# Performance work log

Hardware: AMD Instinct MI355X
Metric: run time of the kernel (lower is better)

## Reference

```python
import jax, jax.numpy as jnp
import numpy as np

BETA = 0.95      # leak
THRESH = 1.0     # snntorch Leaky default threshold
ALPHA = 2.0      # ATan surrogate alpha (atan_with_alpha)
T = 100          # SPIKE_STEPS
D_IN = 65536     # input_dims
HID = 256        # fc1 hidden (hardcoded)
N_OUT = 20       # n_actions(2) * NUM_NEURONS_PER_ACTION(10)


def spike_fn(x):
    # forward of snntorch surrogate.ATan: Heaviside
    return (x > 0.0).astype(x.dtype)


def lif_step(mem, cur):
    # snntorch Leaky, reset_mechanism='subtract':
    # reset computed from previous membrane (detached), then decay+integrate, then fire
    reset = jax.lax.stop_gradient((mem > THRESH).astype(mem.dtype))
    mem_new = BETA * mem + cur - reset * THRESH
    spk = spike_fn(mem_new - THRESH)
    return spk, mem_new


def _run_net(x, W1, b1, W2, b2):
    # x: [T, D_IN]. Precompute all layer-1 currents as one big GEMM, then scan the recurrence.
    cur1_all = x @ W1.T + b1  # [T, HID]

    def step(carry, cur1):
        mem1, mem2 = carry
        spk1, mem1 = lif_step(mem1, cur1)
        cur2 = spk1 @ W2.T + b2  # [n_out]
        spk2, mem2 = lif_step(mem2, cur2)
        return (mem1, mem2), spk2

    init = (jnp.zeros((W1.shape[0],), x.dtype), jnp.zeros((W2.shape[0],), x.dtype))
    (_, mem2_final), spk2_hist = jax.lax.scan(step, init, cur1_all)
    return spk2_hist, mem2_final  # [T, n_out], [n_out]


def setup_inputs() -> dict:
    key = jax.random.key(0)
    ks = jax.random.split(key, 5)
    s = 0.01
    return {
        "poisson_spikes": jax.random.uniform(ks[0], (T, 1, D_IN), dtype=jnp.float32),
        "aW1": jax.random.normal(ks[1], (HID, D_IN), dtype=jnp.float32) * s,
        "ab1": jnp.zeros((HID,), jnp.float32),
        "aW2": jax.random.normal(ks[2], (N_OUT, HID), dtype=jnp.float32) * s,
        "ab2": jnp.zeros((N_OUT,), jnp.float32),
        "cW1": jax.random.normal(ks[3], (HID, D_IN), dtype=jnp.float32) * s,
        "cb1": jnp.zeros((HID,), jnp.float32),
        "cW2": jax.random.normal(ks[4], (1, HID), dtype=jnp.float32) * s,
        "cb2": jnp.zeros((1,), jnp.float32),
    }


def reference(poisson_spikes, aW1, ab1, aW2, ab2, cW1, cb1, cW2, cb2):
    x = poisson_spikes[:, 0, :]  # effective batch of 1 -> [T, D_IN]
    actor_spk_hist, _ = _run_net(x, aW1, ab1, aW2, ab2)        # [T, 20]
    _, critic_mem = _run_net(x, cW1, cb1, cW2, cb2)            # [1]
    spk_sum = actor_spk_hist.sum(axis=0)                       # [20] (sum over timesteps)
    action_vals = jnp.stack([spk_sum[:10].sum(), spk_sum[10:].sum()])
    policy = jax.nn.softmax(action_vals)                       # [2]
    return policy, critic_mem
```

## Files before the change

kernel.cpp:

```cpp
#include <hip/hip_runtime.h>
#include <hip/hip_bf16.h>

#define T_STEPS 100
#define D_IN    65536
#define HID     256
#define HTOT    512
#define BETA    0.95f
#define THRESH  1.0f
#define CHUNK   64
#define ROWS    128

typedef __bf16 bf16x8 __attribute__((ext_vector_type(8)));
typedef float  f32x16 __attribute__((ext_vector_type(16)));

__device__ __forceinline__ void gload_lds16(const float* g, void* l) {
    __builtin_amdgcn_global_load_lds(
        (const __attribute__((address_space(1))) void*)g,
        (__attribute__((address_space(3))) void*)l, 16, 0, 0);
}

__global__ __launch_bounds__(512, 4) void k_gemm1(
    const float* __restrict__ x,
    const float* __restrict__ aW1,
    const float* __restrict__ cW1,
    float* __restrict__ P,
    int Kc)
{
    const int ht   = blockIdx.x;
    const int s    = blockIdx.y;
    const int tid  = threadIdx.x;
    const int lane = tid & 63;
    const int l31  = lane & 31;
    const int wv   = tid >> 6;
    const int wt   = (wv & 1) * 64;
    const int hq   = (wv >> 1) * 32;

    __shared__ __bf16 Ah[ROWS][CHUNK];
    __shared__ __bf16 Am[ROWS][CHUNK];
    __shared__ float  Wf[2][128][32];

    const float* Wbase = (ht < 2) ? (aW1 + (size_t)ht * 128 * D_IN)
                                  : (cW1 + (size_t)(ht - 2) * 128 * D_IN);

    const int gi0   = wv * 64 + lane;
    const int wrow0 = gi0 >> 3,          wg0 = gi0 & 7;
    const int wrow1 = (gi0 + 512) >> 3,  wg1 = (gi0 + 512) & 7;
    const float* wsrc0 = Wbase + (size_t)wrow0 * D_IN + ((wg0 ^ (wrow0 & 7)) * 4);
    const float* wsrc1 = Wbase + (size_t)wrow1 * D_IN + ((wg1 ^ (wrow1 & 7)) * 4);
    char* WfB = (char*)&Wf[0][0][0];

#define WSTAGE(buf, kflt) do {                                                \
    gload_lds16(wsrc0 + (kflt), WfB + (buf) * 16384 + gi0 * 16);              \
    gload_lds16(wsrc1 + (kflt), WfB + (buf) * 16384 + 8192 + gi0 * 16);       \
} while (0)

    const int sr = tid >> 2;
    const int gq = tid & 3;
    const float* xrow = x + (size_t)sr * D_IN + gq * 16;
    const bool xok = (sr < T_STEPS);

#define XSTAGE(kflt) do {                                                     \
    _Pragma("unroll")                                                         \
    for (int j = 0; j < 2; j++) {                                             \
        float4 v0 = make_float4(0.f, 0.f, 0.f, 0.f), v1 = v0;                 \
        if (xok) {                                                            \
            v0 = *(const float4*)(xrow + (kflt) + j * 8);                     \
            v1 = *(const float4*)(xrow + (kflt) + j * 8 + 4);                 \
        }                                                                     \
        float f[8] = {v0.x, v0.y, v0.z, v0.w, v1.x, v1.y, v1.z, v1.w};        \
        bf16x8 hi, mi;                                                        \
        _Pragma("unroll")                                                     \
        for (int e = 0; e < 8; e++) {                                         \
            __bf16 h = (__bf16)f[e];                                          \
            hi[e] = h; mi[e] = (__bf16)(f[e] - (float)h);                     \
        }                                                                     \
        const int slot = gq * 2 + j;                                          \
        const int pe   = ((slot ^ (sr & 7)) << 3);                            \
        *(bf16x8*)&Ah[sr][pe] = hi;                                           \
        *(bf16x8*)&Am[sr][pe] = mi;                                           \
    }                                                                         \
} while (0)

    f32x16 acc0, acc1;
#pragma unroll
    for (int i = 0; i < 16; i++) { acc0[i] = 0.f; acc1[i] = 0.f; }

#define COMPUTE(buf, bk) do {                                                 \
    _Pragma("unroll")                                                         \
    for (int s16 = 0; s16 < 2; s16++) {                                       \
        const int hr = hq + l31;                                              \
        const int gb = s16 * 4 + (lane >> 5) * 2;                             \
        const int g0 = (gb ^ (hr & 7));                                       \
        const int g1 = ((gb + 1) ^ (hr & 7));                                 \
        float4 wa = *(const float4*)&Wf[buf][hr][g0 * 4];                     \
        float4 wb = *(const float4*)&Wf[buf][hr][g1 * 4];                     \
        float fb[8] = {wa.x, wa.y, wa.z, wa.w, wb.x, wb.y, wb.z, wb.w};       \
        bf16x8 bh, bm;                                                        \
        _Pragma("unroll")                                                     \
        for (int e = 0; e < 8; e++) {                                         \
            __bf16 h = (__bf16)fb[e];                                         \
            bh[e] = h; bm[e] = (__bf16)(fb[e] - (float)h);                    \
        }                                                                     \
        const int slot = (bk) * 4 + s16 * 2 + (lane >> 5);                    \
        const int r0 = wt + l31, r1 = r0 + 32;                                \
        const int pe0 = ((slot ^ (r0 & 7)) << 3);                             \
        const int pe1 = ((slot ^ (r1 & 7)) << 3);                             \
        bf16x8 a0h = *(const bf16x8*)&Ah[r0][pe0];                            \
        bf16x8 a0m = *(const bf16x8*)&Am[r0][pe0];                            \
        bf16x8 a1h = *(const bf16x8*)&Ah[r1][pe1];                            \
        bf16x8 a1m = *(const bf16x8*)&Am[r1][pe1];                            \
        acc0 = __builtin_amdgcn_mfma_f32_32x32x16_bf16(a0m, bh, acc0, 0,0,0); \
        acc0 = __builtin_amdgcn_mfma_f32_32x32x16_bf16(a0h, bm, acc0, 0,0,0); \
        acc0 = __builtin_amdgcn_mfma_f32_32x32x16_bf16(a0h, bh, acc0, 0,0,0); \
        acc1 = __builtin_amdgcn_mfma_f32_32x32x16_bf16(a1m, bh, acc1, 0,0,0); \
        acc1 = __builtin_amdgcn_mfma_f32_32x32x16_bf16(a1h, bm, acc1, 0,0,0); \
        acc1 = __builtin_amdgcn_mfma_f32_32x32x16_bf16(a1h, bh, acc1, 0,0,0); \
    }                                                                         \
} while (0)

    const int k0      = s * Kc;
    const int nchunks = Kc / CHUNK;

    WSTAGE(0, k0);
    for (int c = 0; c < nchunks; c++) {
        const int kc = k0 + c * CHUNK;
        asm volatile("s_waitcnt vmcnt(0)" ::: "memory");
        __builtin_amdgcn_s_barrier();
        __builtin_amdgcn_sched_barrier(0);
        XSTAGE(kc);
        asm volatile("s_waitcnt lgkmcnt(0)" ::: "memory");
        __builtin_amdgcn_s_barrier();
        __builtin_amdgcn_sched_barrier(0);
        WSTAGE(1, kc + 32);
        COMPUTE(0, 0);
        asm volatile("s_waitcnt vmcnt(0)" ::: "memory");
        __builtin_amdgcn_s_barrier();
        __builtin_amdgcn_sched_barrier(0);
        if (c + 1 < nchunks) WSTAGE(0, kc + CHUNK);
        COMPUTE(1, 1);
    }
#undef WSTAGE
#undef XSTAGE
#undef COMPUTE

    const int rbase = 4 * (lane >> 5);
    const int hcol  = ht * 128 + hq + l31;
    float* Pb = P + (size_t)s * T_STEPS * HTOT;
#pragma unroll
    for (int reg = 0; reg < 16; reg++) {
        const int row = (reg & 3) + rbase + 8 * (reg >> 2);
        const int t0  = wt + row;
        const int t1  = wt + 32 + row;
        if (t0 < T_STEPS) Pb[(size_t)t0 * HTOT + hcol] = acc0[reg];
        if (t1 < T_STEPS) Pb[(size_t)t1 * HTOT + hcol] = acc1[reg];
    }
}

__global__ __launch_bounds__(256) void k_reduce(
    const float* __restrict__ P,
    const float* __restrict__ ab1, const float* __restrict__ cb1,
    float* __restrict__ cur1, int NS)
{
    int g4 = blockIdx.x * 256 + threadIdx.x;
    int g  = g4 * 4;
    int h0 = g & (HTOT - 1);
    float4 sum;
    sum.x = (h0 + 0 < HID) ? ab1[h0 + 0] : cb1[h0 + 0 - HID];
    sum.y = (h0 + 1 < HID) ? ab1[h0 + 1] : cb1[h0 + 1 - HID];
    sum.z = (h0 + 2 < HID) ? ab1[h0 + 2] : cb1[h0 + 2 - HID];
    sum.w = (h0 + 3 < HID) ? ab1[h0 + 3] : cb1[h0 + 3 - HID];
    for (int ss = 0; ss < NS; ss++) {
        float4 v = *(const float4*)(P + (size_t)ss * T_STEPS * HTOT + g);
        sum.x += v.x; sum.y += v.y; sum.z += v.z; sum.w += v.w;
    }
    *(float4*)(cur1 + g) = sum;
}

__global__ __launch_bounds__(64) void k_lif1(
    const float* __restrict__ cur1,
    unsigned long long* __restrict__ bitsws,
    float* __restrict__ wsa)
{
    const int b    = blockIdx.x;
    const int lane = threadIdx.x;
    const int n    = b * 64 + lane;

    float mem = 0.f;
    for (int tb = 0; tb < T_STEPS; tb += 10) {
        float c[10];
#pragma unroll
        for (int i = 0; i < 10; i++) c[i] = cur1[(size_t)(tb + i) * HTOT + n];
#pragma unroll
        for (int i = 0; i < 10; i++) {
            float reset = (mem > THRESH) ? THRESH : 0.f;
            mem = BETA * mem + c[i] - reset;
            unsigned long long m = __ballot(mem > THRESH);
            if (lane == 0) bitsws[(size_t)(tb + i) * 8 + b] = m;
        }
    }
    if (b == 0 && lane == 0) { wsa[0] = 0.f; wsa[1] = 0.f; }
}

__global__ __launch_bounds__(128) void k_gemm2(
    const unsigned long long* __restrict__ bitsws,
    const float* __restrict__ aW2, const float* __restrict__ ab2,
    const float* __restrict__ cW2, const float* __restrict__ cb2,
    float* __restrict__ wsa, float* __restrict__ out)
{
    const int j   = blockIdx.x;
    const int tid = threadIdx.x;

    __shared__ float W[256];
    __shared__ float c2[T_STEPS];

    const float* Wsrc = (j < 20) ? (aW2 + j * 256) : cW2;
    for (int i = tid; i < 256; i += 128) W[i] = Wsrc[i];
    const float bias  = (j < 20) ? ab2[j] : cb2[0];
    const int   wbase = (j < 20) ? 0 : 4;
    __syncthreads();

    const int t = tid;
    if (t < T_STEPS) {
        unsigned long long m0 = bitsws[(size_t)t * 8 + wbase + 0];
        unsigned long long m1 = bitsws[(size_t)t * 8 + wbase + 1];
        unsigned long long m2 = bitsws[(size_t)t * 8 + wbase + 2];
        unsigned long long m3 = bitsws[(size_t)t * 8 + wbase + 3];
        float acc = bias;
#pragma unroll
        for (int bitp = 0; bitp < 64; bitp++) {
            acc += ((m0 >> bitp) & 1ULL) ? W[bitp]       : 0.f;
            acc += ((m1 >> bitp) & 1ULL) ? W[64 + bitp]  : 0.f;
            acc += ((m2 >> bitp) & 1ULL) ? W[128 + bitp] : 0.f;
            acc += ((m3 >> bitp) & 1ULL) ? W[192 + bitp] : 0.f;
        }
        c2[t] = acc;
    }
    __syncthreads();

    if (tid == 0) {
        float mem = 0.f, spk = 0.f;
        for (int tt = 0; tt < T_STEPS; tt++) {
            float reset = (mem > THRESH) ? THRESH : 0.f;
            mem = BETA * mem + c2[tt] - reset;
            spk += (mem > THRESH) ? 1.f : 0.f;
        }
        if (j < 10)       atomicAdd(&wsa[0], spk);
        else if (j < 20)  atomicAdd(&wsa[1], spk);
        else              out[2] = mem;
    }
}

__global__ __launch_bounds__(64) void k_final(
    const float* __restrict__ wsa, float* __restrict__ out)
{
    if (threadIdx.x == 0) {
        float a0 = wsa[0], a1 = wsa[1];
        float mx = fmaxf(a0, a1);
        float e0 = expf(a0 - mx), e1 = expf(a1 - mx);
        float inv = 1.f / (e0 + e1);
        out[0] = e0 * inv;
        out[1] = e1 * inv;
    }
}

extern "C" void kernel_launch(void* const* d_in, const int* in_sizes, int n_in,
                              void* d_out, int out_size, void* d_ws, size_t ws_size,
                              hipStream_t stream) {
    const float* x   = (const float*)d_in[0];
    const float* aW1 = (const float*)d_in[1];
    const float* ab1 = (const float*)d_in[2];
    const float* aW2 = (const float*)d_in[3];
    const float* ab2 = (const float*)d_in[4];
    const float* cW1 = (const float*)d_in[5];
    const float* cb1 = (const float*)d_in[6];
    const float* cW2 = (const float*)d_in[7];
    const float* cb2 = (const float*)d_in[8];
    float* out = (float*)d_out;

    int NS = 128;
    while (NS > 8 &&
           ((size_t)(NS + 1) * T_STEPS * HTOT) * sizeof(float) + 8192 > ws_size)
        NS >>= 1;
    int Kc = D_IN / NS;

    float* P    = (float*)d_ws;
    float* cur1 = P + (size_t)NS * T_STEPS * HTOT;
    unsigned long long* bitsws =
        (unsigned long long*)(cur1 + T_STEPS * HTOT);
    float* wsa  = (float*)(bitsws + T_STEPS * 8);

    k_gemm1 <<<dim3(4, NS), 512, 0, stream>>>(x, aW1, cW1, P, Kc);
    k_reduce<<<(T_STEPS * HTOT / 4) / 256, 256, 0, stream>>>(P, ab1, cb1, cur1, NS);
    k_lif1  <<<8, 64, 0, stream>>>(cur1, bitsws, wsa);
    k_gemm2 <<<21, 128, 0, stream>>>(bitsws, aW2, ab2, cW2, cb2, wsa, out);
    k_final <<<1, 64, 0, stream>>>(wsa, out);
}
```

Baseline: 97.17 us.

## Pre-pack x into bf16 hi/lo blobs and use a 4-stage async LDS pipeline

Adds a separate kernel that splits x into bf16 high and residual parts once, laid out in swizzled 32-column blobs in workspace. The GEMM1 kernel then streams both the packed x and W through global_load_lds into a 4-deep ring buffer with partial vmcnt waits, replacing the per-block register conversion of x and the double-buffered W. The split count also drops from 128 to 64. This removes redundant x conversion across the four column blocks and overlaps loads with MFMA, at the cost of an extra launch, 32 MB of workspace traffic, and 128 KB of LDS per block, which allows only one block per CU.

```diff
diff --git a/kernel.cpp b/kernel.cpp
--- a/kernel.cpp
+++ b/kernel.cpp
@@ -7,24 +7,50 @@
 #define HTOT    512
 #define BETA    0.95f
 #define THRESH  1.0f
-#define CHUNK   64
-#define ROWS    128
 
 typedef __bf16 bf16x8 __attribute__((ext_vector_type(8)));
 typedef float  f32x16 __attribute__((ext_vector_type(16)));
 
-__device__ __forceinline__ void gload_lds16(const float* g, void* l) {
+__device__ __forceinline__ void gload_lds16(const void* g, void* l) {
     __builtin_amdgcn_global_load_lds(
         (const __attribute__((address_space(1))) void*)g,
         (__attribute__((address_space(3))) void*)l, 16, 0, 0);
 }
 
-__global__ __launch_bounds__(512, 4) void k_gemm1(
-    const float* __restrict__ x,
+__global__ __launch_bounds__(512) void k_xpack(
+    const float* __restrict__ x, __bf16* __restrict__ xp)
+{
+    const int idx  = blockIdx.x * 512 + threadIdx.x;
+    const int slot = idx & 3;
+    const int r    = (idx >> 2) & 127;
+    const int gk   = idx >> 9;
+
+    float f[8] = {0.f, 0.f, 0.f, 0.f, 0.f, 0.f, 0.f, 0.f};
+    if (r < T_STEPS) {
+        const float* src = x + (size_t)r * D_IN + gk * 32 + slot * 8;
+        float4 v0 = *(const float4*)src;
+        float4 v1 = *(const float4*)(src + 4);
+        f[0] = v0.x; f[1] = v0.y; f[2] = v0.z; f[3] = v0.w;
+        f[4] = v1.x; f[5] = v1.y; f[6] = v1.z; f[7] = v1.w;
+    }
+    bf16x8 hi, mi;
+#pragma unroll
+    for (int e = 0; e < 8; e++) {
+        __bf16 h = (__bf16)f[e];
+        hi[e] = h; mi[e] = (__bf16)(f[e] - (float)h);
+    }
+    const int G = r * 4 + (slot ^ ((r >> 1) & 3));
+    __bf16* blob = xp + (size_t)gk * 8192;
+    *(bf16x8*)(blob + G * 8)        = hi;
+    *(bf16x8*)(blob + 4096 + G * 8) = mi;
+}
+
+__global__ __launch_bounds__(512) void k_gemm1(
     const float* __restrict__ aW1,
     const float* __restrict__ cW1,
+    const __bf16* __restrict__ xp,
     float* __restrict__ P,
-    int Kc)
+    int nsteps)
 {
     const int ht   = blockIdx.x;
     const int s    = blockIdx.y;
@@ -35,65 +61,42 @@
     const int wt   = (wv & 1) * 64;
     const int hq   = (wv >> 1) * 32;
 
-    __shared__ __bf16 Ah[ROWS][CHUNK];
-    __shared__ __bf16 Am[ROWS][CHUNK];
-    __shared__ float  Wf[2][128][32];
+    __shared__ __align__(16) char smem[4][32768];
 
     const float* Wbase = (ht < 2) ? (aW1 + (size_t)ht * 128 * D_IN)
                                   : (cW1 + (size_t)(ht - 2) * 128 * D_IN);
 
-    const int gi0   = wv * 64 + lane;
-    const int wrow0 = gi0 >> 3,          wg0 = gi0 & 7;
-    const int wrow1 = (gi0 + 512) >> 3,  wg1 = (gi0 + 512) & 7;
-    const float* wsrc0 = Wbase + (size_t)wrow0 * D_IN + ((wg0 ^ (wrow0 & 7)) * 4);
-    const float* wsrc1 = Wbase + (size_t)wrow1 * D_IN + ((wg1 ^ (wrow1 & 7)) * 4);
-    char* WfB = (char*)&Wf[0][0][0];
-
-#define WSTAGE(buf, kflt) do {                                                \
-    gload_lds16(wsrc0 + (kflt), WfB + (buf) * 16384 + gi0 * 16);              \
-    gload_lds16(wsrc1 + (kflt), WfB + (buf) * 16384 + 8192 + gi0 * 16);       \
+    const int gx0 = wv * 64 + lane;
+    const int gx1 = 512 + gx0;
+    const int wr0 = gx0 >> 3, wj0 = gx0 & 7;
+    const int wr1 = gx1 >> 3, wj1 = gx1 & 7;
+    const float* wsrc0 = Wbase + (size_t)wr0 * D_IN + (wj0 ^ (wr0 & 7)) * 4;
+    const float* wsrc1 = Wbase + (size_t)wr1 * D_IN + (wj1 ^ (wr1 & 7)) * 4;
+    const int gk0 = s * nsteps;
+
+    f32x16 acc0, acc1;
+#pragma unroll
+    for (int i = 0; i < 16; i++) { acc0[i] = 0.f; acc1[i] = 0.f; }
+
+#define STAGE(i) do {                                                         \
+    char* b_ = smem[(i) & 3];                                                 \
+    const __bf16* xb_ = xp + (size_t)(gk0 + (i)) * 8192;                      \
+    const int kc_ = (gk0 + (i)) * 32;                                         \
+    gload_lds16(xb_ + gx0 * 8, b_ + gx0 * 16);                                \
+    gload_lds16(xb_ + gx1 * 8, b_ + gx1 * 16);                                \
+    gload_lds16(wsrc0 + kc_, b_ + 16384 + gx0 * 16);                          \
+    gload_lds16(wsrc1 + kc_, b_ + 16384 + gx1 * 16);                          \
 } while (0)
 
-    const int sr = tid >> 2;
-    const int gq = tid & 3;
-    const float* xrow = x + (size_t)sr * D_IN + gq * 16;
-    const bool xok = (sr < T_STEPS);
-
-#define XSTAGE(kflt) do {                                                     \
-    _Pragma("unroll")                                                         \
-    for (int j = 0; j < 2; j++) {                                             \
-        float4 v0 = make_float4(0.f, 0.f, 0.f, 0.f), v1 = v0;                 \
-        if (xok) {                                                            \
-            v0 = *(const float4*)(xrow + (kflt) + j * 8);                     \
-            v1 = *(const float4*)(xrow + (kflt) + j * 8 + 4);                 \
-        }                                                                     \
-        float f[8] = {v0.x, v0.y, v0.z, v0.w, v1.x, v1.y, v1.z, v1.w};        \
-        bf16x8 hi, mi;                                                        \
-        _Pragma("unroll")                                                     \
-        for (int e = 0; e < 8; e++) {                                         \
-            __bf16 h = (__bf16)f[e];                                          \
-            hi[e] = h; mi[e] = (__bf16)(f[e] - (float)h);                     \
-        }                                                                     \
-        const int slot = gq * 2 + j;                                          \
-        const int pe   = ((slot ^ (sr & 7)) << 3);                            \
-        *(bf16x8*)&Ah[sr][pe] = hi;                                           \
-        *(bf16x8*)&Am[sr][pe] = mi;                                           \
-    }                                                                         \
-} while (0)
-
-    f32x16 acc0, acc1;
-#pragma unroll
-    for (int i = 0; i < 16; i++) { acc0[i] = 0.f; acc1[i] = 0.f; }
-
-#define COMPUTE(buf, bk) do {                                                 \
+#define COMPUTE(i) do {                                                       \
+    const char* b_ = smem[(i) & 3];                                           \
     _Pragma("unroll")                                                         \
     for (int s16 = 0; s16 < 2; s16++) {                                       \
         const int hr = hq + l31;                                              \
         const int gb = s16 * 4 + (lane >> 5) * 2;                             \
-        const int g0 = (gb ^ (hr & 7));                                       \
-        const int g1 = ((gb + 1) ^ (hr & 7));                                 \
-        float4 wa = *(const float4*)&Wf[buf][hr][g0 * 4];                     \
-        float4 wb = *(const float4*)&Wf[buf][hr][g1 * 4];                     \
+        const char* wrow_ = b_ + 16384 + hr * 128;                            \
+        float4 wa = *(const float4*)(wrow_ + ((gb ^ (hr & 7)) * 16));         \
+        float4 wb = *(const float4*)(wrow_ + (((gb + 1) ^ (hr & 7)) * 16));   \
         float fb[8] = {wa.x, wa.y, wa.z, wa.w, wb.x, wb.y, wb.z, wb.w};       \
         bf16x8 bh, bm;                                                        \
         _Pragma("unroll")                                                     \
@@ -101,14 +104,14 @@
             __bf16 h = (__bf16)fb[e];                                         \
             bh[e] = h; bm[e] = (__bf16)(fb[e] - (float)h);                    \
         }                                                                     \
-        const int slot = (bk) * 4 + s16 * 2 + (lane >> 5);                    \
+        const int slot = s16 * 2 + (lane >> 5);                               \
         const int r0 = wt + l31, r1 = r0 + 32;                                \
-        const int pe0 = ((slot ^ (r0 & 7)) << 3);                             \
-        const int pe1 = ((slot ^ (r1 & 7)) << 3);                             \
-        bf16x8 a0h = *(const bf16x8*)&Ah[r0][pe0];                            \
-        bf16x8 a0m = *(const bf16x8*)&Am[r0][pe0];                            \
-        bf16x8 a1h = *(const bf16x8*)&Ah[r1][pe1];                            \
-        bf16x8 a1m = *(const bf16x8*)&Am[r1][pe1];                            \
+        const int G0 = r0 * 4 + (slot ^ ((r0 >> 1) & 3));                     \
+        const int G1 = r1 * 4 + (slot ^ ((r1 >> 1) & 3));                     \
+        bf16x8 a0h = *(const bf16x8*)(b_ + G0 * 16);                          \
+        bf16x8 a0m = *(const bf16x8*)(b_ + 8192 + G0 * 16);                   \
+        bf16x8 a1h = *(const bf16x8*)(b_ + G1 * 16);                          \
+        bf16x8 a1m = *(const bf16x8*)(b_ + 8192 + G1 * 16);                   \
         acc0 = __builtin_amdgcn_mfma_f32_32x32x16_bf16(a0m, bh, acc0, 0,0,0); \
         acc0 = __builtin_amdgcn_mfma_f32_32x32x16_bf16(a0h, bm, acc0, 0,0,0); \
         acc0 = __builtin_amdgcn_mfma_f32_32x32x16_bf16(a0h, bh, acc0, 0,0,0); \
@@ -118,29 +121,20 @@
     }                                                                         \
 } while (0)
 
-    const int k0      = s * Kc;
-    const int nchunks = Kc / CHUNK;
-
-    WSTAGE(0, k0);
-    for (int c = 0; c < nchunks; c++) {
-        const int kc = k0 + c * CHUNK;
-        asm volatile("s_waitcnt vmcnt(0)" ::: "memory");
+    STAGE(0);
+    if (nsteps > 1) STAGE(1);
+    if (nsteps > 2) STAGE(2);
+    for (int i = 0; i < nsteps; i++) {
+        const int rem = nsteps - 1 - i;
+        if (rem >= 2)      asm volatile("s_waitcnt vmcnt(8)" ::: "memory");
+        else if (rem == 1) asm volatile("s_waitcnt vmcnt(4)" ::: "memory");
+        else               asm volatile("s_waitcnt vmcnt(0)" ::: "memory");
         __builtin_amdgcn_s_barrier();
         __builtin_amdgcn_sched_barrier(0);
-        XSTAGE(kc);
-        asm volatile("s_waitcnt lgkmcnt(0)" ::: "memory");
-        __builtin_amdgcn_s_barrier();
-        __builtin_amdgcn_sched_barrier(0);
-        WSTAGE(1, kc + 32);
-        COMPUTE(0, 0);
-        asm volatile("s_waitcnt vmcnt(0)" ::: "memory");
-        __builtin_amdgcn_s_barrier();
-        __builtin_amdgcn_sched_barrier(0);
-        if (c + 1 < nchunks) WSTAGE(0, kc + CHUNK);
-        COMPUTE(1, 1);
-    }
-#undef WSTAGE
-#undef XSTAGE
+        if (i + 3 < nsteps) STAGE(i + 3);
+        COMPUTE(i);
+    }
+#undef STAGE
 #undef COMPUTE
 
     const int rbase = 4 * (lane >> 5);
@@ -277,19 +271,23 @@
     const float* cb2 = (const float*)d_in[8];
     float* out = (float*)d_out;
 
-    int NS = 128;
+    const size_t xpack_bytes = 2048ull * 16384;
+    int NS = 64;
     while (NS > 8 &&
-           ((size_t)(NS + 1) * T_STEPS * HTOT) * sizeof(float) + 8192 > ws_size)
+           xpack_bytes + ((size_t)(NS + 1) * T_STEPS * HTOT) * sizeof(float)
+               + 8192 > ws_size)
         NS >>= 1;
-    int Kc = D_IN / NS;
-
-    float* P    = (float*)d_ws;
-    float* cur1 = P + (size_t)NS * T_STEPS * HTOT;
+    const int nsteps = (D_IN / NS) / 32;
+
+    __bf16* xpack = (__bf16*)d_ws;
+    float*  P     = (float*)((char*)d_ws + xpack_bytes);
+    float*  cur1  = P + (size_t)NS * T_STEPS * HTOT;
     unsigned long long* bitsws =
         (unsigned long long*)(cur1 + T_STEPS * HTOT);
-    float* wsa  = (float*)(bitsws + T_STEPS * 8);
-
-    k_gemm1 <<<dim3(4, NS), 512, 0, stream>>>(x, aW1, cW1, P, Kc);
+    float* wsa = (float*)(bitsws + T_STEPS * 8);
+
+    k_xpack <<<2048, 512, 0, stream>>>(x, xpack);
+    k_gemm1 <<<dim3(4, NS), 512, 0, stream>>>(aW1, cW1, xpack, P, nsteps);
     k_reduce<<<(T_STEPS * HTOT / 4) / 256, 256, 0, stream>>>(P, ab1, cb1, cur1, NS);
     k_lif1  <<<8, 64, 0, stream>>>(cur1, bitsws, wsa);
     k_gemm2 <<<21, 128, 0, stream>>>(bitsws, aW2, ab2, cW2, cb2, wsa, out);
```

Measured after the change: 94.29 us. 1.03x faster.
